# Performance work log

Hardware: AMD Instinct MI355X
Metric: run time of the kernel (lower is better)

The kernel has to match this reference:

```python
import jax, jax.numpy as jnp
import numpy as np

BLOCK = 128  # block_size=(128,128) from MoeFP8Matmul
E, H, I = 8, 2048, 2816  # experts, hidden, intermediate
T, K = 512, 2  # tokens, top-k

_FP8 = getattr(jnp, "float8_e4m3fn", jnp.float32)

def _dequant(w, s):
    # w: [N, Kd] fp8 values (stored fp32), s: [N//128, Kd//128] inverse scales
    s_full = jnp.repeat(jnp.repeat(s, BLOCK, axis=-2), BLOCK, axis=-1)
    return w * s_full

def setup_inputs() -> dict:
    key = jax.random.key(0)
    ks = jax.random.split(key, 7)
    x = jax.random.normal(ks[0], (T, H), dtype=jnp.float32)
    topk_ids = jax.random.randint(ks[1], (T, K), 0, E, dtype=jnp.int64)
    topk_weights = jax.random.uniform(ks[2], (T, K), dtype=jnp.float32)
    # fp8-representable weight values (round-trip through e4m3)
    w13 = (jax.random.normal(ks[3], (E, 2 * I, H), dtype=jnp.float32) * 0.5)
    w13_fp8 = w13.astype(_FP8).astype(jnp.float32)
    w2 = (jax.random.normal(ks[4], (E, H, I), dtype=jnp.float32) * 0.5)
    w2_fp8 = w2.astype(_FP8).astype(jnp.float32)
    w13_scale = jax.random.uniform(ks[5], (E, (2 * I) // BLOCK, H // BLOCK),
                                   dtype=jnp.float32, minval=0.5, maxval=1.5)
    w2_scale = jax.random.uniform(ks[6], (E, H // BLOCK, I // BLOCK),
                                  dtype=jnp.float32, minval=0.5, maxval=1.5)
    return {"x": x, "topk_ids": topk_ids, "topk_weights": topk_weights,
            "w13_fp8": w13_fp8, "w13_scale": w13_scale,
            "w2_fp8": w2_fp8, "w2_scale": w2_scale}

def reference(x, topk_ids, topk_weights, w13_fp8, w13_scale, w2_fp8, w2_scale):
    # Per-expert block-FP8 dequant then grouped SwiGLU MoE GEMM, weighted-summed by router.
    out = jnp.zeros_like(x)
    for e in range(E):  # small fixed expert count
        W13 = _dequant(w13_fp8[e], w13_scale[e])   # [2I, H]
        W2 = _dequant(w2_fp8[e], w2_scale[e])      # [H, I]
        h = x @ W13.T                              # [T, 2I]
        gate, up = jnp.split(h, 2, axis=-1)
        act = jax.nn.silu(gate) * up               # [T, I]
        oe = act @ W2.T                            # [T, H]
        coef = jnp.sum(jnp.where(topk_ids == e, topk_weights, 0.0), axis=-1)  # [T]
        out = out + coef[:, None] * oe
    return out
```

## Files before the change

### kernel.cpp

```cpp
#include <hip/hip_runtime.h>
#include <hip/hip_bf16.h>
#include <cstdint>
#include <cstddef>

#define E_   8
#define H_   2048
#define I_   2816
#define T_   512
#define NPAIR 1024

#define TM   192
#define TN   32
#define BK   64
#define LDSB 72
#define MT_  3

typedef __attribute__((ext_vector_type(8))) short          bf16x8;
typedef __attribute__((ext_vector_type(4))) float          f32x4;
typedef __attribute__((ext_vector_type(8))) unsigned short u16x8;

__device__ __forceinline__ unsigned short f2bf(float f){
  union { float f; unsigned u; } a; a.f = f;
  unsigned u = a.u;
  unsigned r = u + 0x7fffu + ((u >> 16) & 1u);
  return (unsigned short)(r >> 16);
}

__device__ __forceinline__ void cvt4(u16x8& dst, int base, const float4 v, float s){
  __hip_bfloat162 p0 = __float22bfloat162_rn(float2{v.x*s, v.y*s});
  __hip_bfloat162 p1 = __float22bfloat162_rn(float2{v.z*s, v.w*s});
  union { __hip_bfloat162 b; unsigned u; } a0{p0}, a1{p1};
  dst[base+0] = (unsigned short)(a0.u & 0xffff);
  dst[base+1] = (unsigned short)(a0.u >> 16);
  dst[base+2] = (unsigned short)(a1.u & 0xffff);
  dst[base+3] = (unsigned short)(a1.u >> 16);
}

__device__ __forceinline__ void sync_lds(){
  asm volatile("s_waitcnt lgkmcnt(0)\n\ts_barrier" ::: "memory");
}

__global__ void route_kernel(const int* __restrict__ ids,
                             int* __restrict__ offs, int* __restrict__ ptok,
                             int* __restrict__ sop){
  __shared__ int scnt[E_];
  __shared__ int scur[E_];
  const int tid = threadIdx.x;
  if (tid < E_) scnt[tid] = 0;
  __syncthreads();
  const int e = ids[tid];
  atomicAdd(&scnt[e], 1);
  __syncthreads();
  if (tid == 0){
    int s = 0;
    for (int i = 0; i < E_; i++){ offs[i] = s; scur[i] = s; s += scnt[i]; }
    offs[E_] = s;
  }
  __syncthreads();
  const int pos = atomicAdd(&scur[e], 1);
  ptok[pos] = tid >> 1;
  sop[tid]  = pos;
}

__global__ void prep_kernel(const float* __restrict__ x, const int* __restrict__ ptok,
                            unsigned short* __restrict__ xg){
  const int slot = blockIdx.x;
  const int tok  = ptok[slot];
  const int k0   = threadIdx.x * 8;
  const float4 v0 = *(const float4*)(x + (size_t)tok*H_ + k0);
  const float4 v1 = *(const float4*)(x + (size_t)tok*H_ + k0 + 4);
  u16x8 o;
  cvt4(o, 0, v0, 1.f);
  cvt4(o, 4, v1, 1.f);
  *(u16x8*)(xg + (size_t)slot*H_ + k0) = o;
}

__global__ __launch_bounds__(256, 3)
void gemm1_kernel(const unsigned short* __restrict__ xg, const float* __restrict__ w13,
                  const float* __restrict__ s13, const int* __restrict__ offs,
                  unsigned short* __restrict__ act)
{
  const int e   = blockIdx.z;
  const int off = offs[e];
  const int cnt = offs[e+1] - off;
  const int m0  = blockIdx.y * TM;
  if (m0 >= cnt) return;
  const int rows = min(TM, cnt - m0);
  const int nb   = blockIdx.x * TN;

  __shared__ __align__(16) unsigned short Bs[2][2*TN][LDSB];

  const int tid  = threadIdx.x;
  const int wave = tid >> 6;
  const int lane = tid & 63;
  const int quad = lane >> 4;
  const int l16  = lane & 15;

  const float* w13e = w13 + (size_t)e * (2*I_) * H_;
  const float* s13e = s13 + (size_t)e * (2*I_/128) * (H_/128);

  const int br = tid >> 2;
  const int bc = tid & 3;
  const int grow = (br < TN) ? (nb + br) : (I_ + nb + (br - TN));
  const float* bp = w13e + (size_t)grow * H_ + bc*16;
  const int srow  = (((br < TN) ? 0 : (I_/128)) + (nb >> 7)) * (H_/128);

  const unsigned short* aP[MT_];
  #pragma unroll
  for (int mt = 0; mt < MT_; mt++){
    int sl = off + m0 + wave*(TM/4) + mt*16 + l16;
    sl = min(sl, NPAIR - 1);
    aP[mt] = xg + (size_t)sl * H_ + quad*8;
  }

  f32x4 acc[2][MT_][2];
  #pragma unroll
  for (int h = 0; h < 2; h++)
    #pragma unroll
    for (int mt = 0; mt < MT_; mt++)
      #pragma unroll
      for (int nt = 0; nt < 2; nt++)
        acc[h][mt][nt] = (f32x4){0.f, 0.f, 0.f, 0.f};

  float4 R0[4], R1[4];
  bf16x8 A0[2][MT_], A1[2][MT_];
  float  sE, sO;

  auto loadB = [&](int t, float4* R){
    const float* p = bp + t*BK;
    #pragma unroll
    for (int j = 0; j < 4; j++) R[j] = *(const float4*)(p + j*4);
  };
  auto loadA = [&](int t, bf16x8 (*A)[MT_]){
    #pragma unroll
    for (int kk = 0; kk < 2; kk++)
      #pragma unroll
      for (int mt = 0; mt < MT_; mt++)
        A[kk][mt] = *(const bf16x8*)(aP[mt] + t*BK + kk*32);
  };
  auto storeB = [&](const float4* R, float s, int buf){
    u16x8 w0, w1;
    cvt4(w0, 0, R[0], s); cvt4(w0, 4, R[1], s);
    cvt4(w1, 0, R[2], s); cvt4(w1, 4, R[3], s);
    *(u16x8*)&Bs[buf][br][bc*16]     = w0;
    *(u16x8*)&Bs[buf][br][bc*16 + 8] = w1;
  };
  auto mfma = [&](int buf, bf16x8 (*A)[MT_]){
    #pragma unroll
    for (int kk = 0; kk < 2; kk++)
      #pragma unroll
      for (int hh = 0; hh < 2; hh++)
        #pragma unroll
        for (int nt = 0; nt < 2; nt++){
          bf16x8 bv = *(const bf16x8*)&Bs[buf][hh*TN + nt*16 + l16][kk*32 + quad*8];
          #pragma unroll
          for (int mt = 0; mt < MT_; mt++)
            acc[hh][mt][nt] = __builtin_amdgcn_mfma_f32_16x16x32_bf16(A[kk][mt], bv, acc[hh][mt][nt], 0, 0, 0);
        }
  };

  const int NITER = H_/BK;
  loadB(0, R0); sE = s13e[srow];
  loadB(1, R1); sO = s13e[srow];
  loadA(0, A0);
  storeB(R0, sE, 0);
  sync_lds();

  for (int i = 0; i < NITER; i += 2){
    if (i+2 < NITER){ loadB(i+2, R0); sE = s13e[srow + ((i+2) >> 1)]; }
    loadA(i+1, A1);
    mfma(0, A0);
    storeB(R1, sO, 1);
    sync_lds();
    if (i+3 < NITER){ loadB(i+3, R1); sO = s13e[srow + ((i+3) >> 1)]; }
    if (i+2 < NITER) loadA(i+2, A0);
    mfma(1, A1);
    if (i+2 < NITER){ storeB(R0, sE, 0); sync_lds(); }
  }

  #pragma unroll
  for (int mt = 0; mt < MT_; mt++){
    #pragma unroll
    for (int nt = 0; nt < 2; nt++){
      #pragma unroll
      for (int r = 0; r < 4; r++){
        const int m = wave*(TM/4) + mt*16 + quad*4 + r;
        if (m < rows){
          const float g = acc[0][mt][nt][r];
          const float u = acc[1][mt][nt][r];
          const float sg = g / (1.f + __expf(-g));
          act[(size_t)(off + m0 + m)*I_ + (nb + nt*16 + l16)] = f2bf(sg * u);
        }
      }
    }
  }
}

__global__ __launch_bounds__(256, 3)
void gemm2_kernel(const unsigned short* __restrict__ act, const float* __restrict__ w2,
                  const float* __restrict__ s2, const int* __restrict__ offs,
                  float* __restrict__ buf)
{
  const int e   = blockIdx.z;
  const int off = offs[e];
  const int cnt = offs[e+1] - off;
  const int m0  = blockIdx.y * TM;
  if (m0 >= cnt) return;
  const int rows = min(TM, cnt - m0);
  const int nb   = blockIdx.x * TN;

  __shared__ __align__(16) unsigned short Bs[2][TN][LDSB];

  const int tid  = threadIdx.x;
  const int wave = tid >> 6;
  const int lane = tid & 63;
  const int quad = lane >> 4;
  const int l16  = lane & 15;

  const float* w2e = w2 + (size_t)e * H_ * I_;
  const float* s2e = s2 + (size_t)e * (H_/128) * (I_/128);

  const int br = tid >> 3;
  const int bc = tid & 7;
  const float* bp = w2e + (size_t)(nb + br) * I_ + bc*8;
  const int srow  = (nb >> 7) * (I_/128);

  const unsigned short* aP[MT_];
  #pragma unroll
  for (int mt = 0; mt < MT_; mt++){
    int sl = off + m0 + wave*(TM/4) + mt*16 + l16;
    sl = min(sl, NPAIR - 1);
    aP[mt] = act + (size_t)sl * I_ + quad*8;
  }

  f32x4 acc[MT_][2];
  #pragma unroll
  for (int mt = 0; mt < MT_; mt++)
    #pragma unroll
    for (int nt = 0; nt < 2; nt++)
      acc[mt][nt] = (f32x4){0.f, 0.f, 0.f, 0.f};

  float4 R0[2], R1[2];
  bf16x8 A0[2][MT_], A1[2][MT_];
  float  sE, sO;

  auto loadB = [&](int t, float4* R){
    const float* p = bp + t*BK;
    #pragma unroll
    for (int j = 0; j < 2; j++) R[j] = *(const float4*)(p + j*4);
  };
  auto loadA = [&](int t, bf16x8 (*A)[MT_]){
    #pragma unroll
    for (int kk = 0; kk < 2; kk++)
      #pragma unroll
      for (int mt = 0; mt < MT_; mt++)
        A[kk][mt] = *(const bf16x8*)(aP[mt] + t*BK + kk*32);
  };
  auto storeB = [&](const float4* R, float s, int buf_i){
    u16x8 w0;
    cvt4(w0, 0, R[0], s); cvt4(w0, 4, R[1], s);
    *(u16x8*)&Bs[buf_i][br][bc*8] = w0;
  };
  auto mfma = [&](int buf_i, bf16x8 (*A)[MT_]){
    #pragma unroll
    for (int kk = 0; kk < 2; kk++)
      #pragma unroll
      for (int nt = 0; nt < 2; nt++){
        bf16x8 bv = *(const bf16x8*)&Bs[buf_i][nt*16 + l16][kk*32 + quad*8];
        #pragma unroll
        for (int mt = 0; mt < MT_; mt++)
          acc[mt][nt] = __builtin_amdgcn_mfma_f32_16x16x32_bf16(A[kk][mt], bv, acc[mt][nt], 0, 0, 0);
      }
  };

  const int NITER = I_/BK;
  loadB(0, R0); sE = s2e[srow];
  loadB(1, R1); sO = s2e[srow];
  loadA(0, A0);
  storeB(R0, sE, 0);
  sync_lds();

  for (int i = 0; i < NITER; i += 2){
    if (i+2 < NITER){ loadB(i+2, R0); sE = s2e[srow + ((i+2) >> 1)]; }
    loadA(i+1, A1);
    mfma(0, A0);
    storeB(R1, sO, 1);
    sync_lds();
    if (i+3 < NITER){ loadB(i+3, R1); sO = s2e[srow + ((i+3) >> 1)]; }
    if (i+2 < NITER) loadA(i+2, A0);
    mfma(1, A1);
    if (i+2 < NITER){ storeB(R0, sE, 0); sync_lds(); }
  }

  #pragma unroll
  for (int mt = 0; mt < MT_; mt++){
    #pragma unroll
    for (int nt = 0; nt < 2; nt++){
      #pragma unroll
      for (int r = 0; r < 4; r++){
        const int m = wave*(TM/4) + mt*16 + quad*4 + r;
        if (m < rows)
          buf[(size_t)(off + m0 + m)*H_ + (nb + nt*16 + l16)] = acc[mt][nt][r];
      }
    }
  }
}

__global__ void combine_kernel(const float* __restrict__ buf, const int* __restrict__ sop,
                               const float* __restrict__ tw, float* __restrict__ out){
  const int gid = blockIdx.x*256 + threadIdx.x;
  const int t = gid >> 9;
  const int c = gid & 511;
  const int s0 = sop[2*t], s1 = sop[2*t+1];
  const float w0 = tw[2*t], w1 = tw[2*t+1];
  const float4 v0 = ((const float4*)buf)[(size_t)s0*(H_/4) + c];
  const float4 v1 = ((const float4*)buf)[(size_t)s1*(H_/4) + c];
  float4 o;
  o.x = w0*v0.x + w1*v1.x;
  o.y = w0*v0.y + w1*v1.y;
  o.z = w0*v0.z + w1*v1.z;
  o.w = w0*v0.w + w1*v1.w;
  ((float4*)out)[gid] = o;
}

extern "C" void kernel_launch(void* const* d_in, const int* in_sizes, int n_in,
                              void* d_out, int out_size, void* d_ws, size_t ws_size,
                              hipStream_t stream){
  const float* x   = (const float*)d_in[0];
  const int*   ids = (const int*)  d_in[1];
  const float* tw  = (const float*)d_in[2];
  const float* w13 = (const float*)d_in[3];
  const float* s13 = (const float*)d_in[4];
  const float* w2  = (const float*)d_in[5];
  const float* s2  = (const float*)d_in[6];
  float* out = (float*)d_out;

  char* ws = (char*)d_ws;
  int* offs = (int*)ws;
  int* ptok = (int*)(ws + 64);
  int* sop  = (int*)(ws + 64 + 4096);
  unsigned short* xg  = (unsigned short*)(ws + 16384);
  float*          buf = (float*)(ws + 16384);
  unsigned short* act = (unsigned short*)(ws + 16384 + (size_t)NPAIR*H_*4);

  route_kernel  <<<1, NPAIR, 0, stream>>>(ids, offs, ptok, sop);
  prep_kernel   <<<NPAIR, 256, 0, stream>>>(x, ptok, xg);
  gemm1_kernel  <<<dim3(I_/TN, (NPAIR + TM - 1)/TM, E_), 256, 0, stream>>>(xg, w13, s13, offs, act);
  gemm2_kernel  <<<dim3(H_/TN, (NPAIR + TM - 1)/TM, E_), 256, 0, stream>>>(act, w2, s2, offs, buf);
  combine_kernel<<<(T_*H_/4)/256, 256, 0, stream>>>(buf, sop, tw, out);
}
```

Before: 726.1 us.

## Load dequantized weight fragments directly into registers, dropping LDS staging

Both expert GEMM kernels stop staging the dequantized weight tile through double-buffered LDS with barriers. Each wave now loads its fp32 weight fragment straight from global memory, scales it and converts it to bf16 in registers. The N tile is halved to 16 and the occupancy hint is raised to 4 blocks per CU. This removes the LDS writes, LDS reads and barrier stalls. In exchange, all four waves fetch the same weight data, the explicit software prefetch pipeline is gone, and activation rows are re-read across twice as many N tiles.

New measurement: 1.177 ms. 62.0% more time.

```diff
diff --git a/kernel.cpp b/kernel.cpp
--- a/kernel.cpp
+++ b/kernel.cpp
@@ -10,9 +10,8 @@
 #define NPAIR 1024
 
 #define TM   192
-#define TN   32
+#define TN   16
 #define BK   64
-#define LDSB 72
 #define MT_  3
 
 typedef __attribute__((ext_vector_type(8))) short          bf16x8;
@@ -36,8 +35,12 @@
   dst[base+3] = (unsigned short)(a1.u >> 16);
 }
 
-__device__ __forceinline__ void sync_lds(){
-  asm volatile("s_waitcnt lgkmcnt(0)\n\ts_barrier" ::: "memory");
+__device__ __forceinline__ bf16x8 cvt8(const float4 a, const float4 b, float s){
+  u16x8 r;
+  cvt4(r, 0, a, s);
+  cvt4(r, 4, b, s);
+  union { u16x8 u; bf16x8 h; } c; c.u = r;
+  return c.h;
 }
 
 __global__ void route_kernel(const int* __restrict__ ids,
@@ -75,7 +78,7 @@
   *(u16x8*)(xg + (size_t)slot*H_ + k0) = o;
 }
 
-__global__ __launch_bounds__(256, 3)
+__global__ __launch_bounds__(256, 4)
 void gemm1_kernel(const unsigned short* __restrict__ xg, const float* __restrict__ w13,
                   const float* __restrict__ s13, const int* __restrict__ offs,
                   unsigned short* __restrict__ act)
@@ -88,8 +91,6 @@
   const int rows = min(TM, cnt - m0);
   const int nb   = blockIdx.x * TN;
 
-  __shared__ __align__(16) unsigned short Bs[2][2*TN][LDSB];
-
   const int tid  = threadIdx.x;
   const int wave = tid >> 6;
   const int lane = tid & 63;
@@ -99,11 +100,11 @@
   const float* w13e = w13 + (size_t)e * (2*I_) * H_;
   const float* s13e = s13 + (size_t)e * (2*I_/128) * (H_/128);
 
-  const int br = tid >> 2;
-  const int bc = tid & 3;
-  const int grow = (br < TN) ? (nb + br) : (I_ + nb + (br - TN));
-  const float* bp = w13e + (size_t)grow * H_ + bc*16;
-  const int srow  = (((br < TN) ? 0 : (I_/128)) + (nb >> 7)) * (H_/128);
+  const float* bP[2];
+  bP[0] = w13e + (size_t)(nb + l16) * H_ + quad*8;
+  bP[1] = w13e + (size_t)(I_ + nb + l16) * H_ + quad*8;
+  const int sbase0 = (nb >> 7) * (H_/128);
+  const int sbase1 = (I_/128 + (nb >> 7)) * (H_/128);
 
   const unsigned short* aP[MT_];
   #pragma unroll
@@ -113,90 +114,62 @@
     aP[mt] = xg + (size_t)sl * H_ + quad*8;
   }
 
-  f32x4 acc[2][MT_][2];
+  f32x4 acc[2][MT_];
   #pragma unroll
   for (int h = 0; h < 2; h++)
     #pragma unroll
     for (int mt = 0; mt < MT_; mt++)
-      #pragma unroll
-      for (int nt = 0; nt < 2; nt++)
-        acc[h][mt][nt] = (f32x4){0.f, 0.f, 0.f, 0.f};
-
-  float4 R0[4], R1[4];
-  bf16x8 A0[2][MT_], A1[2][MT_];
-  float  sE, sO;
-
-  auto loadB = [&](int t, float4* R){
-    const float* p = bp + t*BK;
-    #pragma unroll
-    for (int j = 0; j < 4; j++) R[j] = *(const float4*)(p + j*4);
-  };
-  auto loadA = [&](int t, bf16x8 (*A)[MT_]){
+      acc[h][mt] = (f32x4){0.f, 0.f, 0.f, 0.f};
+
+  for (int kb = 0; kb < H_; kb += BK){
+    bf16x8 a[2][MT_];
     #pragma unroll
     for (int kk = 0; kk < 2; kk++)
       #pragma unroll
       for (int mt = 0; mt < MT_; mt++)
-        A[kk][mt] = *(const bf16x8*)(aP[mt] + t*BK + kk*32);
-  };
-  auto storeB = [&](const float4* R, float s, int buf){
-    u16x8 w0, w1;
-    cvt4(w0, 0, R[0], s); cvt4(w0, 4, R[1], s);
-    cvt4(w1, 0, R[2], s); cvt4(w1, 4, R[3], s);
-    *(u16x8*)&Bs[buf][br][bc*16]     = w0;
-    *(u16x8*)&Bs[buf][br][bc*16 + 8] = w1;
-  };
-  auto mfma = [&](int buf, bf16x8 (*A)[MT_]){
-    #pragma unroll
-    for (int kk = 0; kk < 2; kk++)
-      #pragma unroll
-      for (int hh = 0; hh < 2; hh++)
+        a[kk][mt] = *(const bf16x8*)(aP[mt] + kb + kk*32);
+
+    float4 b[2][2][2];
+    #pragma unroll
+    for (int hh = 0; hh < 2; hh++)
+      #pragma unroll
+      for (int kk = 0; kk < 2; kk++)
         #pragma unroll
-        for (int nt = 0; nt < 2; nt++){
-          bf16x8 bv = *(const bf16x8*)&Bs[buf][hh*TN + nt*16 + l16][kk*32 + quad*8];
-          #pragma unroll
-          for (int mt = 0; mt < MT_; mt++)
-            acc[hh][mt][nt] = __builtin_amdgcn_mfma_f32_16x16x32_bf16(A[kk][mt], bv, acc[hh][mt][nt], 0, 0, 0);
-        }
-  };
-
-  const int NITER = H_/BK;
-  loadB(0, R0); sE = s13e[srow];
-  loadB(1, R1); sO = s13e[srow];
-  loadA(0, A0);
-  storeB(R0, sE, 0);
-  sync_lds();
-
-  for (int i = 0; i < NITER; i += 2){
-    if (i+2 < NITER){ loadB(i+2, R0); sE = s13e[srow + ((i+2) >> 1)]; }
-    loadA(i+1, A1);
-    mfma(0, A0);
-    storeB(R1, sO, 1);
-    sync_lds();
-    if (i+3 < NITER){ loadB(i+3, R1); sO = s13e[srow + ((i+3) >> 1)]; }
-    if (i+2 < NITER) loadA(i+2, A0);
-    mfma(1, A1);
-    if (i+2 < NITER){ storeB(R0, sE, 0); sync_lds(); }
-  }
-
-  #pragma unroll
-  for (int mt = 0; mt < MT_; mt++){
-    #pragma unroll
-    for (int nt = 0; nt < 2; nt++){
-      #pragma unroll
-      for (int r = 0; r < 4; r++){
-        const int m = wave*(TM/4) + mt*16 + quad*4 + r;
-        if (m < rows){
-          const float g = acc[0][mt][nt][r];
-          const float u = acc[1][mt][nt][r];
-          const float sg = g / (1.f + __expf(-g));
-          act[(size_t)(off + m0 + m)*I_ + (nb + nt*16 + l16)] = f2bf(sg * u);
-        }
+        for (int hf = 0; hf < 2; hf++)
+          b[hh][kk][hf] = *(const float4*)(bP[hh] + kb + kk*32 + hf*4);
+
+    const float s0 = s13e[sbase0 + (kb >> 7)];
+    const float s1 = s13e[sbase1 + (kb >> 7)];
+
+    #pragma unroll
+    for (int kk = 0; kk < 2; kk++){
+      bf16x8 bv0 = cvt8(b[0][kk][0], b[0][kk][1], s0);
+      #pragma unroll
+      for (int mt = 0; mt < MT_; mt++)
+        acc[0][mt] = __builtin_amdgcn_mfma_f32_16x16x32_bf16(a[kk][mt], bv0, acc[0][mt], 0, 0, 0);
+      bf16x8 bv1 = cvt8(b[1][kk][0], b[1][kk][1], s1);
+      #pragma unroll
+      for (int mt = 0; mt < MT_; mt++)
+        acc[1][mt] = __builtin_amdgcn_mfma_f32_16x16x32_bf16(a[kk][mt], bv1, acc[1][mt], 0, 0, 0);
+    }
+  }
+
+  #pragma unroll
+  for (int mt = 0; mt < MT_; mt++){
+    #pragma unroll
+    for (int r = 0; r < 4; r++){
+      const int m = wave*(TM/4) + mt*16 + quad*4 + r;
+      if (m < rows){
+        const float g = acc[0][mt][r];
+        const float u = acc[1][mt][r];
+        const float sg = g / (1.f + __expf(-g));
+        act[(size_t)(off + m0 + m)*I_ + (nb + l16)] = f2bf(sg * u);
       }
     }
   }
 }
 
-__global__ __launch_bounds__(256, 3)
+__global__ __launch_bounds__(256, 4)
 void gemm2_kernel(const unsigned short* __restrict__ act, const float* __restrict__ w2,
                   const float* __restrict__ s2, const int* __restrict__ offs,
                   float* __restrict__ buf)
@@ -209,8 +182,6 @@
   const int rows = min(TM, cnt - m0);
   const int nb   = blockIdx.x * TN;
 
-  __shared__ __align__(16) unsigned short Bs[2][TN][LDSB];
-
   const int tid  = threadIdx.x;
   const int wave = tid >> 6;
   const int lane = tid & 63;
@@ -220,10 +191,8 @@
   const float* w2e = w2 + (size_t)e * H_ * I_;
   const float* s2e = s2 + (size_t)e * (H_/128) * (I_/128);
 
-  const int br = tid >> 3;
-  const int bc = tid & 7;
-  const float* bp = w2e + (size_t)(nb + br) * I_ + bc*8;
-  const int srow  = (nb >> 7) * (I_/128);
+  const float* bP = w2e + (size_t)(nb + l16) * I_ + quad*8;
+  const int sbase = (nb >> 7) * (I_/128);
 
   const unsigned short* aP[MT_];
   #pragma unroll
@@ -233,75 +202,44 @@
     aP[mt] = act + (size_t)sl * I_ + quad*8;
   }
 
-  f32x4 acc[MT_][2];
+  f32x4 acc[MT_];
   #pragma unroll
   for (int mt = 0; mt < MT_; mt++)
-    #pragma unroll
-    for (int nt = 0; nt < 2; nt++)
-      acc[mt][nt] = (f32x4){0.f, 0.f, 0.f, 0.f};
-
-  float4 R0[2], R1[2];
-  bf16x8 A0[2][MT_], A1[2][MT_];
-  float  sE, sO;
-
-  auto loadB = [&](int t, float4* R){
-    const float* p = bp + t*BK;
-    #pragma unroll
-    for (int j = 0; j < 2; j++) R[j] = *(const float4*)(p + j*4);
-  };
-  auto loadA = [&](int t, bf16x8 (*A)[MT_]){
+    acc[mt] = (f32x4){0.f, 0.f, 0.f, 0.f};
+
+  for (int kb = 0; kb < I_; kb += BK){
+    bf16x8 a[2][MT_];
     #pragma unroll
     for (int kk = 0; kk < 2; kk++)
       #pragma unroll
       for (int mt = 0; mt < MT_; mt++)
-        A[kk][mt] = *(const bf16x8*)(aP[mt] + t*BK + kk*32);
-  };
-  auto storeB = [&](const float4* R, float s, int buf_i){
-    u16x8 w0;
-    cvt4(w0, 0, R[0], s); cvt4(w0, 4, R[1], s);
-    *(u16x8*)&Bs[buf_i][br][bc*8] = w0;
-  };
-  auto mfma = [&](int buf_i, bf16x8 (*A)[MT_]){
+        a[kk][mt] = *(const bf16x8*)(aP[mt] + kb + kk*32);
+
+    float4 b[2][2];
     #pragma unroll
     for (int kk = 0; kk < 2; kk++)
       #pragma unroll
-      for (int nt = 0; nt < 2; nt++){
-        bf16x8 bv = *(const bf16x8*)&Bs[buf_i][nt*16 + l16][kk*32 + quad*8];
-        #pragma unroll
-        for (int mt = 0; mt < MT_; mt++)
-          acc[mt][nt] = __builtin_amdgcn_mfma_f32_16x16x32_bf16(A[kk][mt], bv, acc[mt][nt], 0, 0, 0);
-      }
-  };
-
-  const int NITER = I_/BK;
-  loadB(0, R0); sE = s2e[srow];
-  loadB(1, R1); sO = s2e[srow];
-  loadA(0, A0);
-  storeB(R0, sE, 0);
-  sync_lds();
-
-  for (int i = 0; i < NITER; i += 2){
-    if (i+2 < NITER){ loadB(i+2, R0); sE = s2e[srow + ((i+2) >> 1)]; }
-    loadA(i+1, A1);
-    mfma(0, A0);
-    storeB(R1, sO, 1);
-    sync_lds();
-    if (i+3 < NITER){ loadB(i+3, R1); sO = s2e[srow + ((i+3) >> 1)]; }
-    if (i+2 < NITER) loadA(i+2, A0);
-    mfma(1, A1);
-    if (i+2 < NITER){ storeB(R0, sE, 0); sync_lds(); }
-  }
-
-  #pragma unroll
-  for (int mt = 0; mt < MT_; mt++){
-    #pragma unroll
-    for (int nt = 0; nt < 2; nt++){
-      #pragma unroll
-      for (int r = 0; r < 4; r++){
-        const int m = wave*(TM/4) + mt*16 + quad*4 + r;
-        if (m < rows)
-          buf[(size_t)(off + m0 + m)*H_ + (nb + nt*16 + l16)] = acc[mt][nt][r];
-      }
+      for (int hf = 0; hf < 2; hf++)
+        b[kk][hf] = *(const float4*)(bP + kb + kk*32 + hf*4);
+
+    const float s = s2e[sbase + (kb >> 7)];
+
+    #pragma unroll
+    for (int kk = 0; kk < 2; kk++){
+      bf16x8 bv = cvt8(b[kk][0], b[kk][1], s);
+      #pragma unroll
+      for (int mt = 0; mt < MT_; mt++)
+        acc[mt] = __builtin_amdgcn_mfma_f32_16x16x32_bf16(a[kk][mt], bv, acc[mt], 0, 0, 0);
+    }
+  }
+
+  #pragma unroll
+  for (int mt = 0; mt < MT_; mt++){
+    #pragma unroll
+    for (int r = 0; r < 4; r++){
+      const int m = wave*(TM/4) + mt*16 + quad*4 + r;
+      if (m < rows)
+        buf[(size_t)(off + m0 + m)*H_ + (nb + l16)] = acc[mt][r];
     }
   }
 }
```
